# Performance work log

Hardware: AMD Instinct MI355X
Metric: run time of the kernel (lower is better)

Reference implementation:

```python
import jax, jax.numpy as jnp
import numpy as np

N = 10000
F = 256


def setup_inputs() -> dict:
    key = jax.random.key(0)
    k1, k2 = jax.random.split(key)
    x = jax.random.normal(k1, (N, F), dtype=jnp.float32)
    adj = jnp.zeros((N, N), dtype=jnp.float32)  # unused by the module's math
    w = jax.random.normal(k2, (1, 2 * F), dtype=jnp.float32) / np.sqrt(2 * F)
    b = jnp.zeros((1,), dtype=jnp.float32)
    return {"x": x, "adj": adj, "w": w, "b": b}


def reference(x, adj, w, b):
    # Original math: att[i, j] = sigmoid( W @ concat(x[i], x[j]) + b )
    # Split the rank-1 linear: W = [w1 | w2], so
    #   att[i, j] = sigmoid( x[i]@w1 + x[j]@w2 + b )
    # This avoids materializing the O(n^2, 2F) gather/concat intermediate.
    f = x.shape[1]
    w1 = w[0, :f]   # [F]
    w2 = w[0, f:]   # [F]
    s1 = x @ w1     # [N]
    s2 = x @ w2     # [N]
    att = jax.nn.sigmoid(s1[:, None] + s2[None, :] + b[0])  # [N, N]
    return att
```

## Files before the change

### kernel.cpp

```cpp
#include <hip/hip_runtime.h>
#include <hip/hip_bf16.h>

#define N_ROWS 10000
#define F_DIM 256
#define J4 (N_ROWS / 4)

__global__ void dot_kernel(const float* __restrict__ x,
                           const float* __restrict__ w,
                           const float* __restrict__ b,
                           float* __restrict__ s1b,
                           float* __restrict__ s2) {
    const int row = blockIdx.x;
    const int t = threadIdx.x;
    const float xv = x[(size_t)row * F_DIM + t];
    float p1 = xv * w[t];
    float p2 = xv * w[F_DIM + t];
    #pragma unroll
    for (int o = 32; o > 0; o >>= 1) {
        p1 += __shfl_down(p1, o);
        p2 += __shfl_down(p2, o);
    }
    __shared__ float a1[4], a2[4];
    const int wid = t >> 6;
    if ((t & 63) == 0) { a1[wid] = p1; a2[wid] = p2; }
    __syncthreads();
    if (t == 0) {
        s1b[row] = (a1[0] + a1[1] + a1[2] + a1[3]) + b[0];
        s2[row]  = (a2[0] + a2[1] + a2[2] + a2[3]);
    }
}

__device__ __forceinline__ float sigmoidf(float z) {
    return 1.0f / (1.0f + __expf(-z));
}

__global__ void att_kernel(const float* __restrict__ s1b,
                           const float* __restrict__ s2,
                           float* __restrict__ out) {
    const int row = blockIdx.y;
    const int j4 = blockIdx.x * blockDim.x + threadIdx.x;
    if (j4 >= J4) return;
    const float a = s1b[row];
    float4 v = reinterpret_cast<const float4*>(s2)[j4];
    float4 r;
    r.x = sigmoidf(a + v.x);
    r.y = sigmoidf(a + v.y);
    r.z = sigmoidf(a + v.z);
    r.w = sigmoidf(a + v.w);
    reinterpret_cast<float4*>(out)[(size_t)row * J4 + j4] = r;
}

extern "C" void kernel_launch(void* const* d_in, const int* in_sizes, int n_in,
                              void* d_out, int out_size, void* d_ws, size_t ws_size,
                              hipStream_t stream) {
    const float* x = (const float*)d_in[0];
    const float* w = (const float*)d_in[2];
    const float* b = (const float*)d_in[3];
    float* out = (float*)d_out;

    float* s1b = (float*)d_ws;
    float* s2  = s1b + N_ROWS;

    dot_kernel<<<N_ROWS, F_DIM, 0, stream>>>(x, w, b, s1b, s2);

    dim3 grid((J4 + 255) / 256, N_ROWS);
    att_kernel<<<grid, 256, 0, stream>>>(s1b, s2, out);
}
```

Baseline: 86.71 us.

## Factor sigmoid exponent per row/column and write four rows per thread

Computes exp(-s1-b) and exp(-s2) once per row/column in the dot kernel, so each output element needs only one fma and a fast reciprocal instead of an exp and a divide. The dot kernel now gives each wavefront one row using float4 loads and no shared memory. The att kernel writes four output rows per thread with nontemporal stores, reusing the e2 vector load. The product of two exponentials can overflow to inf for large scores, and the fast rcp lowers precision slightly.

```diff
diff --git a/kernel.cpp b/kernel.cpp
--- a/kernel.cpp
+++ b/kernel.cpp
@@ -4,50 +4,52 @@
 #define N_ROWS 10000
 #define F_DIM 256
 #define J4 (N_ROWS / 4)
+#define LOG2E 1.44269504088896340736f
+
+typedef float f32x4 __attribute__((ext_vector_type(4)));
 
 __global__ void dot_kernel(const float* __restrict__ x,
                            const float* __restrict__ w,
                            const float* __restrict__ b,
-                           float* __restrict__ s1b,
-                           float* __restrict__ s2) {
-    const int row = blockIdx.x;
-    const int t = threadIdx.x;
-    const float xv = x[(size_t)row * F_DIM + t];
-    float p1 = xv * w[t];
-    float p2 = xv * w[F_DIM + t];
+                           float* __restrict__ e1,
+                           float* __restrict__ e2) {
+    const int wid  = threadIdx.x >> 6;
+    const int lane = threadIdx.x & 63;
+    const int row  = blockIdx.x * 4 + wid;
+    const f32x4 xv = reinterpret_cast<const f32x4*>(x + (size_t)row * F_DIM)[lane];
+    const f32x4 w1 = reinterpret_cast<const f32x4*>(w)[lane];
+    const f32x4 w2 = reinterpret_cast<const f32x4*>(w + F_DIM)[lane];
+    float p1 = xv.x * w1.x + xv.y * w1.y + xv.z * w1.z + xv.w * w1.w;
+    float p2 = xv.x * w2.x + xv.y * w2.y + xv.z * w2.z + xv.w * w2.w;
     #pragma unroll
     for (int o = 32; o > 0; o >>= 1) {
-        p1 += __shfl_down(p1, o);
-        p2 += __shfl_down(p2, o);
+        p1 += __shfl_xor(p1, o);
+        p2 += __shfl_xor(p2, o);
     }
-    __shared__ float a1[4], a2[4];
-    const int wid = t >> 6;
-    if ((t & 63) == 0) { a1[wid] = p1; a2[wid] = p2; }
-    __syncthreads();
-    if (t == 0) {
-        s1b[row] = (a1[0] + a1[1] + a1[2] + a1[3]) + b[0];
-        s2[row]  = (a2[0] + a2[1] + a2[2] + a2[3]);
+    if (lane == 0) {
+        e1[row] = __builtin_amdgcn_exp2f(-(p1 + b[0]) * LOG2E);
+        e2[row] = __builtin_amdgcn_exp2f(-p2 * LOG2E);
     }
 }
 
-__device__ __forceinline__ float sigmoidf(float z) {
-    return 1.0f / (1.0f + __expf(-z));
-}
-
-__global__ void att_kernel(const float* __restrict__ s1b,
-                           const float* __restrict__ s2,
+__global__ void att_kernel(const float* __restrict__ e1,
+                           const float* __restrict__ e2,
                            float* __restrict__ out) {
-    const int row = blockIdx.y;
     const int j4 = blockIdx.x * blockDim.x + threadIdx.x;
     if (j4 >= J4) return;
-    const float a = s1b[row];
-    float4 v = reinterpret_cast<const float4*>(s2)[j4];
-    float4 r;
-    r.x = sigmoidf(a + v.x);
-    r.y = sigmoidf(a + v.y);
-    r.z = sigmoidf(a + v.z);
-    r.w = sigmoidf(a + v.w);
-    reinterpret_cast<float4*>(out)[(size_t)row * J4 + j4] = r;
+    const int i0 = blockIdx.y * 4;
+    const f32x4 ev = reinterpret_cast<const f32x4*>(e2)[j4];
+    #pragma unroll
+    for (int r = 0; r < 4; ++r) {
+        const float a = e1[i0 + r];
+        f32x4 o;
+        o.x = __builtin_amdgcn_rcpf(fmaf(a, ev.x, 1.0f));
+        o.y = __builtin_amdgcn_rcpf(fmaf(a, ev.y, 1.0f));
+        o.z = __builtin_amdgcn_rcpf(fmaf(a, ev.z, 1.0f));
+        o.w = __builtin_amdgcn_rcpf(fmaf(a, ev.w, 1.0f));
+        __builtin_nontemporal_store(
+            o, reinterpret_cast<f32x4*>(out) + (size_t)(i0 + r) * J4 + j4);
+    }
 }
 
 extern "C" void kernel_launch(void* const* d_in, const int* in_sizes, int n_in,
@@ -58,11 +60,11 @@
     const float* b = (const float*)d_in[3];
     float* out = (float*)d_out;
 
-    float* s1b = (float*)d_ws;
-    float* s2  = s1b + N_ROWS;
+    float* e1 = (float*)d_ws;
+    float* e2 = e1 + N_ROWS;
 
-    dot_kernel<<<N_ROWS, F_DIM, 0, stream>>>(x, w, b, s1b, s2);
+    dot_kernel<<<N_ROWS / 4, 256, 0, stream>>>(x, w, b, e1, e2);
 
-    dim3 grid((J4 + 255) / 256, N_ROWS);
-    att_kernel<<<grid, 256, 0, stream>>>(s1b, s2, out);
+    dim3 grid((J4 + 255) / 256, N_ROWS / 4);
+    att_kernel<<<grid, 256, 0, stream>>>(e1, e2, out);
 }
```

After: 82.67 us, median of 2. 4.7% less time.
